# Kernel optimization log

Measured on AMD Instinct MI355X. Metric: run time of the kernel, lower is better.

The kernel has to match this reference:

```python
import jax, jax.numpy as jnp
import numpy as np

B, N, D = 64, 32, 512

# Off-diagonal pair indices in the exact order the torch module uses:
# k = N*i + j for i in range(N) for j in range(N) if j != i.
_pairs = [(i, j) for i in range(N) for j in range(N) if j != i]
IDX_I = jnp.asarray(np.array([p[0] for p in _pairs], dtype=np.int32))  # [N*(N-1)]
IDX_J = jnp.asarray(np.array([p[1] for p in _pairs], dtype=np.int32))


def setup_inputs() -> dict:
    key = jax.random.key(0)
    k0, k1, k2 = jax.random.split(key, 3)
    person_feats = jax.random.normal(k0, (B, N, D), dtype=jnp.float32)
    # MLP: Linear(2D -> D) -> ReLU -> Linear(D -> D); Kaiming-ish scaling.
    W1 = jax.random.normal(k1, (D, 2 * D), dtype=jnp.float32) * (1.0 / np.sqrt(2 * D))
    b1 = jnp.zeros((D,), dtype=jnp.float32)
    W2 = jax.random.normal(k2, (D, D), dtype=jnp.float32) * (1.0 / np.sqrt(D))
    b2 = jnp.zeros((D,), dtype=jnp.float32)
    return {"person_feats": person_feats, "W1": W1, "b1": b1, "W2": W2, "b2": b2}


def reference(person_feats, W1, b1, W2, b2):
    # Original math: tem1[b, N*i+j] = feats[b, i]; tem2[b, N*i+j] = feats[b, j];
    # select off-diagonal indices -> pairwise concat(feat_i, feat_j).
    # We gather the N*(N-1) needed pairs directly instead of materializing N*N.
    fi = person_feats[:, IDX_I, :]            # [B, N*(N-1), D]
    fj = person_feats[:, IDX_J, :]            # [B, N*(N-1), D]
    x = jnp.concatenate([fi, fj], axis=-1)    # [B, N*(N-1), 2D]
    h = jax.nn.relu(jnp.einsum('bpk,dk->bpd', x, W1) + b1)
    out = jnp.einsum('bpk,dk->bpd', h, W2) + b2  # [B, N*(N-1), D]
    return out
```

## Files before the change

### kernel.cpp

```cpp
#include <hip/hip_runtime.h>
#include <hip/hip_bf16.h>
#include <stdint.h>


typedef __attribute__((ext_vector_type(4))) float f32x4;
typedef __attribute__((ext_vector_type(8))) short bf16x8;
typedef __attribute__((ext_vector_type(4))) unsigned int u32x4;

__device__ __forceinline__ uint32_t cvt2_bf16(float a, float b) {
    __hip_bfloat162 h = __float22bfloat162_rn(make_float2(a, b));
    uint32_t u;
    __builtin_memcpy(&u, &h, 4);
    return u;
}

__device__ __forceinline__ void async_lds16(const void* g, void* l) {
    __builtin_amdgcn_global_load_lds(
        (const __attribute__((address_space(1))) void*)g,
        (__attribute__((address_space(3))) void*)l, 16, 0, 0);
}

__global__ __launch_bounds__(256) void prep(const float* __restrict__ pf,
                                            const float* __restrict__ W1,
                                            const float* __restrict__ b1,
                                            const float* __restrict__ W2,
                                            float* __restrict__ UV,
                                            unsigned short* __restrict__ W2r) {
    __shared__ unsigned short As[32][64];
    __shared__ unsigned short Bs[128][64];

    const int t = threadIdx.x;
    const int bxg = blockIdx.x;

    if (bxg >= 512) {
        int s = (bxg - 512) * 256 + t;
        int l = s & 63;
        int fn = (s >> 6) & 31;
        int kt = s >> 11;
        int col = fn * 16 + (l & 15);
        int k = kt * 32 + (l >> 4) * 8;
        const float* src = W2 + (size_t)col * 512 + k;
        f32x4 a = ((const f32x4*)src)[0];
        f32x4 b = ((const f32x4*)src)[1];
        u32x4 P;
        P[0] = cvt2_bf16(a[0], a[1]); P[1] = cvt2_bf16(a[2], a[3]);
        P[2] = cvt2_bf16(b[0], b[1]); P[3] = cvt2_bf16(b[2], b[3]);
        *(u32x4*)(W2r + (size_t)s * 8) = P;
        return;
    }

    const int m0 = (bxg >> 3) * 32;
    const int c0 = (bxg & 7) * 128;

    const int row8 = t >> 3;
    const int g = t & 7;

    const int wave = t >> 6, lane = t & 63;
    const int wr = wave >> 1, wc = wave & 1;
    const int lr = lane & 15, lkq = lane >> 4;
    const int s7 = lr & 7;

    f32x4 acc[4] = {};

    const float* a_src = pf + (size_t)(m0 + row8) * 512 + g * 8;
    const float* b_src[4];
    int wbB[4];
#pragma unroll
    for (int p = 0; p < 4; ++p) {
        int rb = p * 32 + row8;
        int c = c0 + rb;
        int d = c & 511;
        int koff = (c >> 9) * 512;
        b_src[p] = W1 + (size_t)d * 1024 + koff + g * 8;
        wbB[p] = rb * 128 + ((g ^ (rb & 7)) << 4);
    }
    const int wbA = row8 * 128 + ((g ^ (row8 & 7)) << 4);

    for (int kt = 0; kt < 512; kt += 64) {
        {
            const float* gp = a_src + kt;
            f32x4 x0 = ((const f32x4*)gp)[0];
            f32x4 x1 = ((const f32x4*)gp)[1];
            u32x4 P;
            P[0] = cvt2_bf16(x0[0], x0[1]); P[1] = cvt2_bf16(x0[2], x0[3]);
            P[2] = cvt2_bf16(x1[0], x1[1]); P[3] = cvt2_bf16(x1[2], x1[3]);
            *(u32x4*)((char*)&As[0][0] + wbA) = P;
        }
#pragma unroll
        for (int p = 0; p < 4; ++p) {
            const float* gp = b_src[p] + kt;
            f32x4 x0 = ((const f32x4*)gp)[0];
            f32x4 x1 = ((const f32x4*)gp)[1];
            u32x4 P;
            P[0] = cvt2_bf16(x0[0], x0[1]); P[1] = cvt2_bf16(x0[2], x0[3]);
            P[2] = cvt2_bf16(x1[0], x1[1]); P[3] = cvt2_bf16(x1[2], x1[3]);
            *(u32x4*)((char*)&Bs[0][0] + wbB[p]) = P;
        }
        __syncthreads();
#pragma unroll
        for (int kk = 0; kk < 2; ++kk) {
            const int co = (((kk << 2) + lkq) ^ s7) << 3;
            bf16x8 af = *(const bf16x8*)(&As[0][0] + (wr * 16 + lr) * 64 + co);
#pragma unroll
            for (int n = 0; n < 4; ++n) {
                bf16x8 bfr = *(const bf16x8*)(&Bs[0][0] + (wc * 64 + n * 16 + lr) * 64 + co);
                acc[n] = __builtin_amdgcn_mfma_f32_16x16x32_bf16(af, bfr, acc[n], 0, 0, 0);
            }
        }
        __syncthreads();
    }

    const int cr = lane >> 4;
    const int cc = lane & 15;
#pragma unroll
    for (int n = 0; n < 4; ++n) {
        int c = c0 + wc * 64 + n * 16 + cc;
        float bias = (c < 512) ? b1[c] : 0.0f;
        int rowb = m0 + wr * 16 + cr * 4;
#pragma unroll
        for (int r_ = 0; r_ < 4; ++r_)
            UV[(size_t)(rowb + r_) * 1024 + c] = acc[n][r_] + bias;
    }
}

__global__ __launch_bounds__(256, 2) void fused_gemm(const float* __restrict__ UV,
                                                     const unsigned short* __restrict__ W2r,
                                                     const float* __restrict__ b2,
                                                     float* __restrict__ out) {
    __shared__ unsigned char As[2][4096];
    __shared__ unsigned char Bs[2][32768];

    const int t = threadIdx.x;
    const int bx = blockIdx.x;
    const int mt = (bx & 7) * 124 + (bx >> 3);
    const int m0 = mt << 6;

    const int wave = t >> 6, lane = t & 63;

    const int arow = t >> 2;
    const int ks = t & 3;
    const float* uptr;
    const float* vptr;
    {
        int m = m0 + arow;
        int b = m / 992, p = m - b * 992;
        int i = p / 31, r = p - i * 31;
        int j = r + (r >= i ? 1 : 0);
        uptr = UV + (size_t)(b * 32 + i) * 1024 + ks * 8;
        vptr = UV + (size_t)(b * 32 + j) * 1024 + 512 + ks * 8;
    }
    const int awoff = (arow >> 4) * 1024 + (ks * 16 + (arow & 15)) * 16;

    const int cr = lane >> 4;
    const int cc = lane & 15;

    f32x4 acc[8][4] = {};

    f32x4 Pu0, Pu1, Pv0, Pv1;
    f32x4 Qu0, Qu1, Qv0, Qv1;

#define DMA_B(S, DSTBUF)                                                       \
    {                                                                          \
        const char* gs = (const char*)W2r + (S) * 32768 + t * 16;              \
        _Pragma("unroll")                                                      \
        for (int q = 0; q < 8; ++q)                                            \
            async_lds16(gs + q * 4096, &Bs[DSTBUF][0] + q * 4096 + wave * 1024);\
    }

#define LOAD_UV(S, U0, U1, V0, V1)                                             \
    {                                                                          \
        const float* up = uptr + (S) * 32;                                     \
        const float* vp = vptr + (S) * 32;                                     \
        U0 = ((const f32x4*)up)[0]; U1 = ((const f32x4*)up)[1];                \
        V0 = ((const f32x4*)vp)[0]; V1 = ((const f32x4*)vp)[1];                \
    }

#define BUILD_A(DSTBUF, U0, U1, V0, V1)                                        \
    {                                                                          \
        f32x4 h0, h1;                                                          \
        _Pragma("unroll")                                                      \
        for (int q = 0; q < 4; ++q) {                                          \
            h0[q] = fmaxf(U0[q] + V0[q], 0.0f);                                \
            h1[q] = fmaxf(U1[q] + V1[q], 0.0f);                                \
        }                                                                      \
        u32x4 P;                                                               \
        P[0] = cvt2_bf16(h0[0], h0[1]); P[1] = cvt2_bf16(h0[2], h0[3]);        \
        P[2] = cvt2_bf16(h1[0], h1[1]); P[3] = cvt2_bf16(h1[2], h1[3]);        \
        *(u32x4*)(&As[DSTBUF][0] + awoff) = P;                                 \
    }

#define MFMA_STEP(BUF)                                                         \
    {                                                                          \
        const unsigned char* aB = &As[BUF][0];                                 \
        const unsigned char* bB = &Bs[BUF][0];                                 \
        bf16x8 af[4], bfr[8];                                                  \
        _Pragma("unroll")                                                      \
        for (int m = 0; m < 4; ++m)                                            \
            af[m] = *(const bf16x8*)(aB + m * 1024 + lane * 16);               \
        _Pragma("unroll")                                                      \
        for (int n = 0; n < 8; ++n)                                            \
            bfr[n] = *(const bf16x8*)(bB + (wave * 8 + n) * 1024 + lane * 16); \
        __builtin_amdgcn_s_setprio(1);                                         \
        _Pragma("unroll")                                                      \
        for (int n = 0; n < 8; ++n)                                            \
            _Pragma("unroll")                                                  \
            for (int m = 0; m < 4; ++m)                                        \
                acc[n][m] = __builtin_amdgcn_mfma_f32_16x16x32_bf16(           \
                    af[m], bfr[n], acc[n][m], 0, 0, 0);                        \
        __builtin_amdgcn_s_setprio(0);                                         \
    }

    DMA_B(0, 0);
    LOAD_UV(0, Pu0, Pu1, Pv0, Pv1);
    LOAD_UV(1, Qu0, Qu1, Qv0, Qv1);
    BUILD_A(0, Pu0, Pu1, Pv0, Pv1);

#pragma unroll 1
    for (int s2 = 0; s2 < 16; s2 += 2) {
        __syncthreads();
        DMA_B(s2 + 1, 1);
        if (s2 < 14) LOAD_UV(s2 + 2, Pu0, Pu1, Pv0, Pv1);
        MFMA_STEP(0);
        BUILD_A(1, Qu0, Qu1, Qv0, Qv1);

        __syncthreads();
        if (s2 < 14) DMA_B(s2 + 2, 0);
        if (s2 < 14) LOAD_UV(s2 + 3, Qu0, Qu1, Qv0, Qv1);
        MFMA_STEP(1);
        if (s2 < 14) BUILD_A(0, Pu0, Pu1, Pv0, Pv1);
    }
#undef DMA_B
#undef LOAD_UV
#undef BUILD_A
#undef MFMA_STEP

#pragma unroll
    for (int n = 0; n < 8; ++n) {
        int col = wave * 128 + n * 16 + cc;
        float bias = b2[col];
#pragma unroll
        for (int m = 0; m < 4; ++m) {
            int rowb = m0 + m * 16 + cr * 4;
#pragma unroll
            for (int r_ = 0; r_ < 4; ++r_)
                out[(size_t)(rowb + r_) * 512 + col] = acc[n][m][r_] + bias;
        }
    }
}

extern "C" void kernel_launch(void* const* d_in, const int* in_sizes, int n_in,
                              void* d_out, int out_size, void* d_ws, size_t ws_size,
                              hipStream_t stream) {
    const float* pf = (const float*)d_in[0];
    const float* W1 = (const float*)d_in[1];
    const float* b1 = (const float*)d_in[2];
    const float* W2 = (const float*)d_in[3];
    const float* b2 = (const float*)d_in[4];
    float* out = (float*)d_out;

    float* UV = (float*)d_ws;
    unsigned short* W2r = (unsigned short*)((char*)d_ws + (size_t)8 * 1024 * 1024);

    prep<<<dim3(640), dim3(256), 0, stream>>>(pf, W1, b1, W2, UV, W2r);
    fused_gemm<<<dim3(992), dim3(256), 0, stream>>>(UV, W2r, b2, out);
}
```

Before: 78.96 us.

## Double threads per block in fused GEMM, halving per-wave output tile

Launches the second GEMM with 512 threads (8 waves) instead of 256, so each wave computes 64 output columns instead of 128 and holds half the accumulators. A-tile construction and B-tile DMA work are split across twice as many threads, with each thread loading 4 floats of U/V instead of 8. The aim is more waves in flight to hide latency, with lower register pressure per wave. In exchange each wave does fewer MFMAs per A-fragment load, so A-fragments are read from LDS more often and barriers cover more waves.

```diff
diff --git a/kernel.cpp b/kernel.cpp
--- a/kernel.cpp
+++ b/kernel.cpp
@@ -6,6 +6,7 @@
 typedef __attribute__((ext_vector_type(4))) float f32x4;
 typedef __attribute__((ext_vector_type(8))) short bf16x8;
 typedef __attribute__((ext_vector_type(4))) unsigned int u32x4;
+typedef __attribute__((ext_vector_type(2))) unsigned int u32x2;
 
 __device__ __forceinline__ uint32_t cvt2_bf16(float a, float b) {
     __hip_bfloat162 h = __float22bfloat162_rn(make_float2(a, b));
@@ -123,7 +124,7 @@
     }
 }
 
-__global__ __launch_bounds__(256, 2) void fused_gemm(const float* __restrict__ UV,
+__global__ __launch_bounds__(512, 2) void fused_gemm(const float* __restrict__ UV,
                                                      const unsigned short* __restrict__ W2r,
                                                      const float* __restrict__ b2,
                                                      float* __restrict__ out) {
@@ -137,8 +138,8 @@
 
     const int wave = t >> 6, lane = t & 63;
 
-    const int arow = t >> 2;
-    const int ks = t & 3;
+    const int arow = t >> 3;
+    const int ksl = t & 7;
     const float* uptr;
     const float* vptr;
     {
@@ -146,63 +147,58 @@
         int b = m / 992, p = m - b * 992;
         int i = p / 31, r = p - i * 31;
         int j = r + (r >= i ? 1 : 0);
-        uptr = UV + (size_t)(b * 32 + i) * 1024 + ks * 8;
-        vptr = UV + (size_t)(b * 32 + j) * 1024 + 512 + ks * 8;
-    }
-    const int awoff = (arow >> 4) * 1024 + (ks * 16 + (arow & 15)) * 16;
+        uptr = UV + (size_t)(b * 32 + i) * 1024 + ksl * 4;
+        vptr = UV + (size_t)(b * 32 + j) * 1024 + 512 + ksl * 4;
+    }
+    const int awoff = (arow >> 4) * 1024 + (((ksl >> 1) * 16 + (arow & 15)) << 4)
+                    + ((ksl & 1) << 3);
 
     const int cr = lane >> 4;
     const int cc = lane & 15;
 
-    f32x4 acc[8][4] = {};
-
-    f32x4 Pu0, Pu1, Pv0, Pv1;
-    f32x4 Qu0, Qu1, Qv0, Qv1;
+    f32x4 acc[4][4] = {};
+
+    f32x4 Pu, Pv;
+    f32x4 Qu, Qv;
 
 #define DMA_B(S, DSTBUF)                                                       \
     {                                                                          \
         const char* gs = (const char*)W2r + (S) * 32768 + t * 16;              \
         _Pragma("unroll")                                                      \
-        for (int q = 0; q < 8; ++q)                                            \
-            async_lds16(gs + q * 4096, &Bs[DSTBUF][0] + q * 4096 + wave * 1024);\
-    }
-
-#define LOAD_UV(S, U0, U1, V0, V1)                                             \
-    {                                                                          \
-        const float* up = uptr + (S) * 32;                                     \
-        const float* vp = vptr + (S) * 32;                                     \
-        U0 = ((const f32x4*)up)[0]; U1 = ((const f32x4*)up)[1];                \
-        V0 = ((const f32x4*)vp)[0]; V1 = ((const f32x4*)vp)[1];                \
-    }
-
-#define BUILD_A(DSTBUF, U0, U1, V0, V1)                                        \
-    {                                                                          \
-        f32x4 h0, h1;                                                          \
-        _Pragma("unroll")                                                      \
-        for (int q = 0; q < 4; ++q) {                                          \
-            h0[q] = fmaxf(U0[q] + V0[q], 0.0f);                                \
-            h1[q] = fmaxf(U1[q] + V1[q], 0.0f);                                \
-        }                                                                      \
-        u32x4 P;                                                               \
-        P[0] = cvt2_bf16(h0[0], h0[1]); P[1] = cvt2_bf16(h0[2], h0[3]);        \
-        P[2] = cvt2_bf16(h1[0], h1[1]); P[3] = cvt2_bf16(h1[2], h1[3]);        \
-        *(u32x4*)(&As[DSTBUF][0] + awoff) = P;                                 \
+        for (int q = 0; q < 4; ++q)                                            \
+            async_lds16(gs + q * 8192, &Bs[DSTBUF][0] + q * 8192 + wave * 1024);\
+    }
+
+#define LOAD_UV(S, U0, V0)                                                     \
+    {                                                                          \
+        U0 = *(const f32x4*)(uptr + (S) * 32);                                 \
+        V0 = *(const f32x4*)(vptr + (S) * 32);                                 \
+    }
+
+#define BUILD_A(DSTBUF, U0, V0)                                                \
+    {                                                                          \
+        f32x4 h;                                                               \
+        _Pragma("unroll")                                                      \
+        for (int q = 0; q < 4; ++q) h[q] = fmaxf(U0[q] + V0[q], 0.0f);         \
+        u32x2 P;                                                               \
+        P[0] = cvt2_bf16(h[0], h[1]); P[1] = cvt2_bf16(h[2], h[3]);            \
+        *(u32x2*)(&As[DSTBUF][0] + awoff) = P;                                 \
     }
 
 #define MFMA_STEP(BUF)                                                         \
     {                                                                          \
         const unsigned char* aB = &As[BUF][0];                                 \
         const unsigned char* bB = &Bs[BUF][0];                                 \
-        bf16x8 af[4], bfr[8];                                                  \
+        bf16x8 af[4], bfr[4];                                                  \
         _Pragma("unroll")                                                      \
         for (int m = 0; m < 4; ++m)                                            \
             af[m] = *(const bf16x8*)(aB + m * 1024 + lane * 16);               \
         _Pragma("unroll")                                                      \
-        for (int n = 0; n < 8; ++n)                                            \
-            bfr[n] = *(const bf16x8*)(bB + (wave * 8 + n) * 1024 + lane * 16); \
+        for (int n = 0; n < 4; ++n)                                            \
+            bfr[n] = *(const bf16x8*)(bB + (wave * 4 + n) * 1024 + lane * 16); \
         __builtin_amdgcn_s_setprio(1);                                         \
         _Pragma("unroll")                                                      \
-        for (int n = 0; n < 8; ++n)                                            \
+        for (int n = 0; n < 4; ++n)                                            \
             _Pragma("unroll")                                                  \
             for (int m = 0; m < 4; ++m)                                        \
                 acc[n][m] = __builtin_amdgcn_mfma_f32_16x16x32_bf16(           \
@@ -211,23 +207,23 @@
     }
 
     DMA_B(0, 0);
-    LOAD_UV(0, Pu0, Pu1, Pv0, Pv1);
-    LOAD_UV(1, Qu0, Qu1, Qv0, Qv1);
-    BUILD_A(0, Pu0, Pu1, Pv0, Pv1);
+    LOAD_UV(0, Pu, Pv);
+    LOAD_UV(1, Qu, Qv);
+    BUILD_A(0, Pu, Pv);
 
 #pragma unroll 1
     for (int s2 = 0; s2 < 16; s2 += 2) {
         __syncthreads();
         DMA_B(s2 + 1, 1);
-        if (s2 < 14) LOAD_UV(s2 + 2, Pu0, Pu1, Pv0, Pv1);
+        if (s2 < 14) LOAD_UV(s2 + 2, Pu, Pv);
         MFMA_STEP(0);
-        BUILD_A(1, Qu0, Qu1, Qv0, Qv1);
+        BUILD_A(1, Qu, Qv);
 
         __syncthreads();
         if (s2 < 14) DMA_B(s2 + 2, 0);
-        if (s2 < 14) LOAD_UV(s2 + 3, Qu0, Qu1, Qv0, Qv1);
+        if (s2 < 14) LOAD_UV(s2 + 3, Qu, Qv);
         MFMA_STEP(1);
-        if (s2 < 14) BUILD_A(0, Pu0, Pu1, Pv0, Pv1);
+        if (s2 < 14) BUILD_A(0, Pu, Pv);
     }
 #undef DMA_B
 #undef LOAD_UV
@@ -235,8 +231,8 @@
 #undef MFMA_STEP
 
 #pragma unroll
-    for (int n = 0; n < 8; ++n) {
-        int col = wave * 128 + n * 16 + cc;
+    for (int n = 0; n < 4; ++n) {
+        int col = wave * 64 + n * 16 + cc;
         float bias = b2[col];
 #pragma unroll
         for (int m = 0; m < 4; ++m) {
@@ -262,5 +258,5 @@
     unsigned short* W2r = (unsigned short*)((char*)d_ws + (size_t)8 * 1024 * 1024);
 
     prep<<<dim3(640), dim3(256), 0, stream>>>(pf, W1, b1, W2, UV, W2r);
-    fused_gemm<<<dim3(992), dim3(256), 0, stream>>>(UV, W2r, b2, out);
-}
+    fused_gemm<<<dim3(992), dim3(512), 0, stream>>>(UV, W2r, b2, out);
+}
```

After: 100.7 us. +27.6%, slower.

## Load W2 fragments directly from global into registers, drop LDS staging for B

Applied to the files above, without the earlier changes.

The B operand (pre-packed W2) is no longer copied into a 64KB LDS double buffer with async global-to-LDS loads. Each wave now loads its own fragments straight into double-buffered registers, and the barrier becomes a custom s_waitcnt lgkmcnt(0) plus s_barrier that does not wait on global loads. This frees LDS and drops the LDS reads per step, which may allow higher occupancy. The cost is more VGPR pressure from the 16 extra bf16x8 registers and exposed global latency. The inline-asm barrier does not wait on vmcnt, so correctness relies on the compiler inserting waits before the B registers are used.

```diff
diff --git a/kernel.cpp b/kernel.cpp
--- a/kernel.cpp
+++ b/kernel.cpp
@@ -12,12 +12,6 @@
     uint32_t u;
     __builtin_memcpy(&u, &h, 4);
     return u;
-}
-
-__device__ __forceinline__ void async_lds16(const void* g, void* l) {
-    __builtin_amdgcn_global_load_lds(
-        (const __attribute__((address_space(1))) void*)g,
-        (__attribute__((address_space(3))) void*)l, 16, 0, 0);
 }
 
 __global__ __launch_bounds__(256) void prep(const float* __restrict__ pf,
@@ -128,7 +122,6 @@
                                                      const float* __restrict__ b2,
                                                      float* __restrict__ out) {
     __shared__ unsigned char As[2][4096];
-    __shared__ unsigned char Bs[2][32768];
 
     const int t = threadIdx.x;
     const int bx = blockIdx.x;
@@ -151,6 +144,9 @@
     }
     const int awoff = (arow >> 4) * 1024 + (ks * 16 + (arow & 15)) * 16;
 
+    const unsigned char* bsrc = (const unsigned char*)W2r +
+                                (size_t)(wave * 8) * 1024 + lane * 16;
+
     const int cr = lane >> 4;
     const int cc = lane & 15;
 
@@ -158,13 +154,14 @@
 
     f32x4 Pu0, Pu1, Pv0, Pv1;
     f32x4 Qu0, Qu1, Qv0, Qv1;
-
-#define DMA_B(S, DSTBUF)                                                       \
-    {                                                                          \
-        const char* gs = (const char*)W2r + (S) * 32768 + t * 16;              \
-        _Pragma("unroll")                                                      \
-        for (int q = 0; q < 8; ++q)                                            \
-            async_lds16(gs + q * 4096, &Bs[DSTBUF][0] + q * 4096 + wave * 1024);\
+    bf16x8 Bp[8], Bq[8];
+
+#define LOAD_B(S, DST)                                                         \
+    {                                                                          \
+        const unsigned char* gb = bsrc + (size_t)(S) * 32768;                  \
+        _Pragma("unroll")                                                      \
+        for (int n = 0; n < 8; ++n)                                            \
+            DST[n] = *(const bf16x8*)(gb + n * 1024);                          \
     }
 
 #define LOAD_UV(S, U0, U1, V0, V1)                                             \
@@ -189,50 +186,49 @@
         *(u32x4*)(&As[DSTBUF][0] + awoff) = P;                                 \
     }
 
-#define MFMA_STEP(BUF)                                                         \
+#define MFMA_STEP(BUF, BREG)                                                   \
     {                                                                          \
         const unsigned char* aB = &As[BUF][0];                                 \
-        const unsigned char* bB = &Bs[BUF][0];                                 \
-        bf16x8 af[4], bfr[8];                                                  \
+        bf16x8 af[4];                                                          \
         _Pragma("unroll")                                                      \
         for (int m = 0; m < 4; ++m)                                            \
             af[m] = *(const bf16x8*)(aB + m * 1024 + lane * 16);               \
-        _Pragma("unroll")                                                      \
-        for (int n = 0; n < 8; ++n)                                            \
-            bfr[n] = *(const bf16x8*)(bB + (wave * 8 + n) * 1024 + lane * 16); \
         __builtin_amdgcn_s_setprio(1);                                         \
         _Pragma("unroll")                                                      \
         for (int n = 0; n < 8; ++n)                                            \
             _Pragma("unroll")                                                  \
             for (int m = 0; m < 4; ++m)                                        \
                 acc[n][m] = __builtin_amdgcn_mfma_f32_16x16x32_bf16(           \
-                    af[m], bfr[n], acc[n][m], 0, 0, 0);                        \
+                    af[m], BREG[n], acc[n][m], 0, 0, 0);                       \
         __builtin_amdgcn_s_setprio(0);                                         \
     }
 
-    DMA_B(0, 0);
+#define BARRIER() asm volatile("s_waitcnt lgkmcnt(0)\n\ts_barrier" ::: "memory")
+
+    LOAD_B(0, Bp);
     LOAD_UV(0, Pu0, Pu1, Pv0, Pv1);
     LOAD_UV(1, Qu0, Qu1, Qv0, Qv1);
     BUILD_A(0, Pu0, Pu1, Pv0, Pv1);
 
 #pragma unroll 1
     for (int s2 = 0; s2 < 16; s2 += 2) {
-        __syncthreads();
-        DMA_B(s2 + 1, 1);
+        BARRIER();
+        LOAD_B(s2 + 1, Bq);
         if (s2 < 14) LOAD_UV(s2 + 2, Pu0, Pu1, Pv0, Pv1);
-        MFMA_STEP(0);
+        MFMA_STEP(0, Bp);
         BUILD_A(1, Qu0, Qu1, Qv0, Qv1);
 
-        __syncthreads();
-        if (s2 < 14) DMA_B(s2 + 2, 0);
+        BARRIER();
+        if (s2 < 14) LOAD_B(s2 + 2, Bp);
         if (s2 < 14) LOAD_UV(s2 + 3, Qu0, Qu1, Qv0, Qv1);
-        MFMA_STEP(1);
+        MFMA_STEP(1, Bq);
         if (s2 < 14) BUILD_A(0, Pu0, Pu1, Pv0, Pv1);
     }
-#undef DMA_B
+#undef LOAD_B
 #undef LOAD_UV
 #undef BUILD_A
 #undef MFMA_STEP
+#undef BARRIER
 
 #pragma unroll
     for (int n = 0; n < 8; ++n) {
```

Result: faster. 73.40 us (-7.0%).
